# Kernel tuning notes

Measured on AMD Instinct MI355X. Metric: run time of the kernel, lower is better.

Reference implementation:

```python
import jax, jax.numpy as jnp
import numpy as np

HEAD = 16
EMB = 1024
D_K = EMB // HEAD


def setup_inputs() -> dict:
    key = jax.random.key(0)
    ks = jax.random.split(key, 11)
    B, S, E = 2, 2048, EMB
    scale = 1.0 / np.sqrt(E)
    inp = {
        "query": jax.random.normal(ks[0], (B, S, E), jnp.float32),
        "key": jax.random.normal(ks[1], (B, S, E), jnp.float32),
        "value": jax.random.normal(ks[2], (B, S, E), jnp.float32),
        "Wq": jax.random.normal(ks[3], (E, E), jnp.float32) * scale,
        "bq": jnp.zeros((E,), jnp.float32),
        "Wk": jax.random.normal(ks[4], (E, E), jnp.float32) * scale,
        "bk": jnp.zeros((E,), jnp.float32),
        "Wv": jax.random.normal(ks[5], (E, E), jnp.float32) * scale,
        "bv": jnp.zeros((E,), jnp.float32),
        "Wo": jax.random.normal(ks[6], (E, E), jnp.float32) * scale,
        "bo": jnp.zeros((E,), jnp.float32),
    }
    return inp


def reference(query, key, value, Wq, bq, Wk, bk, Wv, bv, Wo, bo):
    B, S, E = query.shape
    # 3 input projections, split into heads: [B, H, S, d_k]
    def proj(x, W, b):
        return (x @ W.T + b).reshape(B, S, HEAD, D_K).transpose(0, 2, 1, 3)

    q = proj(query, Wq, bq)
    k = proj(key, Wk, bk)
    v = proj(value, Wv, bv)

    # scaled dot-product attention (full matrix, as in original)
    scores = jnp.einsum("bhqd,bhkd->bhqk", q, k) / jnp.sqrt(jnp.float32(D_K))
    attn = jax.nn.softmax(scores, axis=-1)  # dropout in eval mode = identity
    x = jnp.einsum("bhqk,bhkd->bhqd", attn, v)

    # merge heads and output projection
    x = x.transpose(0, 2, 1, 3).reshape(B, S, E)
    return x @ Wo.T + bo
```

## Files before the change

kernel.cpp:

```cpp
#include <hip/hip_runtime.h>
#include <hip/hip_bf16.h>
#include <math.h>


constexpr int Sn = 2048;
constexpr int En = 1024;
constexpr int Hn = 16;
constexpr int Dk = 64;
constexpr int Kn = 1024;
constexpr size_t WSZ = 1048576;
constexpr size_t TSZ = 4194304;
constexpr int PST = 72;

#define QSCALE 0.18033688011112042f

typedef __bf16 bf16x8 __attribute__((ext_vector_type(8)));
typedef float  f32x4  __attribute__((ext_vector_type(4)));

union U16 { uint4 u; bf16x8 v; __hip_bfloat16 h[8]; };
union U8  { uint2 u; __hip_bfloat162 h2[2]; __hip_bfloat16 h[4]; };

__device__ inline U16 cvt8f(const float* __restrict__ p) {
    float4 a = *(const float4*)p;
    float4 b = *(const float4*)(p + 4);
    U16 r;
    r.h[0] = __float2bfloat16(a.x); r.h[1] = __float2bfloat16(a.y);
    r.h[2] = __float2bfloat16(a.z); r.h[3] = __float2bfloat16(a.w);
    r.h[4] = __float2bfloat16(b.x); r.h[5] = __float2bfloat16(b.y);
    r.h[6] = __float2bfloat16(b.z); r.h[7] = __float2bfloat16(b.w);
    return r;
}

__device__ inline void gload16(const __hip_bfloat16* g, __hip_bfloat16* l) {
    __builtin_amdgcn_global_load_lds(
        (const __attribute__((address_space(1))) void*)g,
        (__attribute__((address_space(3))) void*)l, 16, 0, 0);
}

template<int ROWS, int NW>
__device__ inline void stage_tile(const __hip_bfloat16* __restrict__ src, int ld,
                                  __hip_bfloat16* lds, int w, int lane) {
    int l8 = lane >> 3;
    int g = (lane & 7) ^ (l8 & 7);
    #pragma unroll
    for (int j = 0; j < ROWS / (8 * NW); ++j) {
        int c = j * NW + w;
        gload16(src + (size_t)(c * 8 + l8) * ld + g * 8, lds + c * 512);
    }
}

__global__ __launch_bounds__(256)
void cvt_w(const float* __restrict__ w0, const float* __restrict__ w1,
           const float* __restrict__ w2, const float* __restrict__ w3,
           __hip_bfloat16* __restrict__ dst)
{
    int y = blockIdx.y;
    const float* src = (y == 0) ? w0 : (y == 1) ? w1 : (y == 2) ? w2 : w3;
    size_t i = ((size_t)blockIdx.x * 256 + threadIdx.x) * 8;
    U16 r = cvt8f(src + i);
    *(uint4*)&dst[(size_t)y * WSZ + i] = r.u;
}

__global__ __launch_bounds__(256)
void cvt_x3(const float* __restrict__ q, const float* __restrict__ k,
            const float* __restrict__ v, __hip_bfloat16* __restrict__ dst)
{
    int z = blockIdx.y;
    const float* src = (z == 0) ? q : (z == 1) ? k : v;
    size_t i = ((size_t)blockIdx.x * 256 + threadIdx.x) * 8;
    U16 r = cvt8f(src + i);
    *(uint4*)&dst[(size_t)z * TSZ + i] = r.u;
}

template<int NT>
__device__ inline void gemm_core(const __hip_bfloat16* __restrict__ Ab,
                                 const __hip_bfloat16* __restrict__ Wb,
                                 __hip_bfloat16* As, __hip_bfloat16* Bs,
                                 f32x4 (&acc)[2][NT], int w, int lane)
{
    const int l15 = lane & 15, lg = lane >> 4, l7 = lane & 7;
    const int wm = (w & 1) * 32, wn = (w >> 1) * (NT * 16);
    const int coff0 = (lg ^ l7) * 8;
    const int coff1 = ((4 + lg) ^ l7) * 8;

    #pragma unroll
    for (int i = 0; i < 2; ++i)
        #pragma unroll
        for (int j = 0; j < NT; ++j) acc[i][j] = {0.f, 0.f, 0.f, 0.f};

    for (int k0 = 0; k0 < Kn; k0 += 64) {
        stage_tile<64, 4>(Ab + k0, Kn, As, w, lane);
        stage_tile<NT * 32, 4>(Wb + k0, Kn, Bs, w, lane);
        __syncthreads();

        U16 af[2][2], bf[NT][2];
        #pragma unroll
        for (int mt = 0; mt < 2; ++mt) {
            int r = (wm + mt * 16 + l15) * 64;
            af[mt][0].u = *(const uint4*)&As[r + coff0];
            af[mt][1].u = *(const uint4*)&As[r + coff1];
        }
        #pragma unroll
        for (int nt = 0; nt < NT; ++nt) {
            int r = (wn + nt * 16 + l15) * 64;
            bf[nt][0].u = *(const uint4*)&Bs[r + coff0];
            bf[nt][1].u = *(const uint4*)&Bs[r + coff1];
        }
        #pragma unroll
        for (int mt = 0; mt < 2; ++mt)
            #pragma unroll
            for (int nt = 0; nt < NT; ++nt) {
                acc[mt][nt] = __builtin_amdgcn_mfma_f32_16x16x32_bf16(af[mt][0].v, bf[nt][0].v, acc[mt][nt], 0, 0, 0);
                acc[mt][nt] = __builtin_amdgcn_mfma_f32_16x16x32_bf16(af[mt][1].v, bf[nt][1].v, acc[mt][nt], 0, 0, 0);
            }
        __syncthreads();
    }
}

__global__ __launch_bounds__(256)
void gemm_qkv(const __hip_bfloat16* __restrict__ X, const __hip_bfloat16* __restrict__ Wall,
              const float* __restrict__ bq, const float* __restrict__ bk,
              const float* __restrict__ bv, __hip_bfloat16* __restrict__ outbase)
{
    __shared__ __align__(16) __hip_bfloat16 As[64 * 64];
    __shared__ __align__(16) __hip_bfloat16 Bs[128 * 64];

    const int tid = threadIdx.x, w = tid >> 6, lane = tid & 63;
    const int z = blockIdx.z;
    const int blockM = blockIdx.x * 64, blockN = blockIdx.y * 128;

    f32x4 acc[2][4];
    gemm_core<4>(X + (size_t)z * TSZ + (size_t)blockM * Kn,
                 Wall + (size_t)z * WSZ + (size_t)blockN * Kn,
                 As, Bs, acc, w, lane);

    const float scale = (z == 0) ? QSCALE : 1.0f;
    const float* bias = (z == 0) ? bq : (z == 1) ? bk : bv;
    __hip_bfloat16* out = outbase + (size_t)z * TSZ;

    const int l15 = lane & 15, lg = lane >> 4;
    const int wm = (w & 1) * 32, wn = (w >> 1) * 64;

    #pragma unroll
    for (int nt = 0; nt < 4; ++nt) {
        int n = blockN + wn + nt * 16 + l15;
        float bvn = bias[n] * scale;
        int h_ = n >> 6, d_ = n & 63;
        #pragma unroll
        for (int mt = 0; mt < 2; ++mt) {
            int m0 = blockM + wm + mt * 16 + lg * 4;
            int b_ = m0 >> 11, s_ = m0 & (Sn - 1);
            if (z < 2) {
                #pragma unroll
                for (int i = 0; i < 4; ++i)
                    out[(((size_t)b_ * Hn + h_) * Sn + s_ + i) * Dk + d_] =
                        __float2bfloat16(fmaf(acc[mt][nt][i], scale, bvn));
            } else {
                U8 pk;
                #pragma unroll
                for (int i = 0; i < 4; ++i)
                    pk.h[i] = __float2bfloat16(fmaf(acc[mt][nt][i], scale, bvn));
                *(uint2*)&out[(((size_t)b_ * Hn + h_) * Dk + d_) * Sn + s_] = pk.u;
            }
        }
    }
}

__global__ __launch_bounds__(256)
void gemm_out(const __hip_bfloat16* __restrict__ A, const __hip_bfloat16* __restrict__ W,
              const float* __restrict__ bias, float* __restrict__ out)
{
    __shared__ __align__(16) __hip_bfloat16 As[64 * 64];
    __shared__ __align__(16) __hip_bfloat16 Bs[64 * 64];

    const int tid = threadIdx.x, w = tid >> 6, lane = tid & 63;
    const int blockM = blockIdx.x * 64, blockN = blockIdx.y * 64;

    f32x4 acc[2][2];
    gemm_core<2>(A + (size_t)blockM * Kn, W + (size_t)blockN * Kn,
                 As, Bs, acc, w, lane);

    const int l15 = lane & 15, lg = lane >> 4;
    const int wm = (w & 1) * 32, wn = (w >> 1) * 32;

    #pragma unroll
    for (int nt = 0; nt < 2; ++nt) {
        int n = blockN + wn + nt * 16 + l15;
        float bvn = bias[n];
        #pragma unroll
        for (int mt = 0; mt < 2; ++mt) {
            int m0 = blockM + wm + mt * 16 + lg * 4;
            #pragma unroll
            for (int i = 0; i < 4; ++i)
                out[(size_t)(m0 + i) * Kn + n] = acc[mt][nt][i] + bvn;
        }
    }
}

__global__ __launch_bounds__(256)
void attn(const __hip_bfloat16* __restrict__ Q, const __hip_bfloat16* __restrict__ K,
          const __hip_bfloat16* __restrict__ Vt, __hip_bfloat16* __restrict__ X)
{
    __shared__ __align__(16) __hip_bfloat16 Ks[2][64 * 64];
    __shared__ __align__(16) __hip_bfloat16 Vts[2][64 * 64];
    __shared__ __align__(16) __hip_bfloat16 Ps[128 * PST];

    const int bh = blockIdx.y, q0 = blockIdx.x * 128;
    const int tid = threadIdx.x, w = tid >> 6, lane = tid & 63;
    const int l15 = lane & 15, lg = lane >> 4, l7 = lane & 7;
    const int coff0 = (lg ^ l7) * 8;
    const int coff1 = ((4 + lg) ^ l7) * 8;

    const __hip_bfloat16* Qb = Q  + (size_t)bh * Sn * Dk;
    const __hip_bfloat16* Kb = K  + (size_t)bh * Sn * Dk;
    const __hip_bfloat16* Vb = Vt + (size_t)bh * Dk * Sn;

    U16 aq[2][2];
    #pragma unroll
    for (int qt = 0; qt < 2; ++qt) {
        const __hip_bfloat16* qp = Qb + (size_t)(q0 + w * 32 + qt * 16 + l15) * Dk + lg * 8;
        aq[qt][0].u = *(const uint4*)qp;
        aq[qt][1].u = *(const uint4*)(qp + 32);
    }

    f32x4 o[2][4];
    float lpart[2];
    #pragma unroll
    for (int qt = 0; qt < 2; ++qt) {
        lpart[qt] = 0.f;
        #pragma unroll
        for (int dt = 0; dt < 4; ++dt) o[qt][dt] = {0.f, 0.f, 0.f, 0.f};
    }

    __hip_bfloat16* Pw = Ps + (w * 32) * PST;

    stage_tile<64, 4>(Kb, Dk, Ks[0], w, lane);
    stage_tile<64, 4>(Vb, Sn, Vts[0], w, lane);

    for (int t = 0; t < Sn / 64; ++t) {
        __syncthreads();
        const int cur = t & 1;
        if (t + 1 < Sn / 64) {
            stage_tile<64, 4>(Kb + (size_t)(t + 1) * 64 * Dk, Dk, Ks[cur ^ 1], w, lane);
            stage_tile<64, 4>(Vb + (t + 1) * 64, Sn, Vts[cur ^ 1], w, lane);
        }

        U16 kf[4][2];
        #pragma unroll
        for (int kt = 0; kt < 4; ++kt) {
            int r = (kt * 16 + l15) * 64;
            kf[kt][0].u = *(const uint4*)&Ks[cur][r + coff0];
            kf[kt][1].u = *(const uint4*)&Ks[cur][r + coff1];
        }
        #pragma unroll
        for (int kt = 0; kt < 4; ++kt)
            #pragma unroll
            for (int qt = 0; qt < 2; ++qt) {
                f32x4 s = {0.f, 0.f, 0.f, 0.f};
                s = __builtin_amdgcn_mfma_f32_16x16x32_bf16(kf[kt][0].v, aq[qt][0].v, s, 0, 0, 0);
                s = __builtin_amdgcn_mfma_f32_16x16x32_bf16(kf[kt][1].v, aq[qt][1].v, s, 0, 0, 0);
                float p0 = __builtin_amdgcn_exp2f(s[0]), p1 = __builtin_amdgcn_exp2f(s[1]);
                float p2 = __builtin_amdgcn_exp2f(s[2]), p3 = __builtin_amdgcn_exp2f(s[3]);
                lpart[qt] += (p0 + p1) + (p2 + p3);
                U8 pk;
                pk.h2[0] = __float22bfloat162_rn({p0, p1});
                pk.h2[1] = __float22bfloat162_rn({p2, p3});
                *(uint2*)&Pw[(qt * 16 + l15) * PST + kt * 16 + lg * 4] = pk.u;
            }

        U16 pf[2][2], vf[4][2];
        #pragma unroll
        for (int qt = 0; qt < 2; ++qt) {
            const __hip_bfloat16* pr = &Pw[(qt * 16 + l15) * PST + lg * 8];
            pf[qt][0].u = *(const uint4*)pr;
            pf[qt][1].u = *(const uint4*)(pr + 32);
        }
        #pragma unroll
        for (int dt = 0; dt < 4; ++dt) {
            int r = (dt * 16 + l15) * 64;
            vf[dt][0].u = *(const uint4*)&Vts[cur][r + coff0];
            vf[dt][1].u = *(const uint4*)&Vts[cur][r + coff1];
        }
        #pragma unroll
        for (int qt = 0; qt < 2; ++qt)
            #pragma unroll
            for (int dt = 0; dt < 4; ++dt) {
                o[qt][dt] = __builtin_amdgcn_mfma_f32_16x16x32_bf16(pf[qt][0].v, vf[dt][0].v, o[qt][dt], 0, 0, 0);
                o[qt][dt] = __builtin_amdgcn_mfma_f32_16x16x32_bf16(pf[qt][1].v, vf[dt][1].v, o[qt][dt], 0, 0, 0);
            }
    }

    float linv[2][4];
    #pragma unroll
    for (int qt = 0; qt < 2; ++qt) {
        float v = lpart[qt];
        v += __shfl_xor(v, 16, 64);
        v += __shfl_xor(v, 32, 64);
        #pragma unroll
        for (int i = 0; i < 4; ++i)
            linv[qt][i] = 1.f / __shfl(v, lg * 4 + i, 16);
    }

    int b_ = bh >> 4, h_ = bh & (Hn - 1);
    #pragma unroll
    for (int qt = 0; qt < 2; ++qt)
        #pragma unroll
        for (int i = 0; i < 4; ++i) {
            int sr = q0 + w * 32 + qt * 16 + lg * 4 + i;
            __hip_bfloat16* xp = X + ((size_t)(b_ * Sn + sr)) * En + h_ * Dk + l15;
            #pragma unroll
            for (int dt = 0; dt < 4; ++dt)
                xp[dt * 16] = __float2bfloat16(o[qt][dt][i] * linv[qt][i]);
        }
}

extern "C" void kernel_launch(void* const* d_in, const int* in_sizes, int n_in,
                              void* d_out, int out_size, void* d_ws, size_t ws_size,
                              hipStream_t stream)
{
    const float* query = (const float*)d_in[0];
    const float* key   = (const float*)d_in[1];
    const float* value = (const float*)d_in[2];
    const float* Wq = (const float*)d_in[3];
    const float* bq = (const float*)d_in[4];
    const float* Wk = (const float*)d_in[5];
    const float* bk = (const float*)d_in[6];
    const float* Wv = (const float*)d_in[7];
    const float* bv = (const float*)d_in[8];
    const float* Wo = (const float*)d_in[9];
    const float* bo = (const float*)d_in[10];
    float* out = (float*)d_out;

    __hip_bfloat16* xqkv = (__hip_bfloat16*)d_ws;
    __hip_bfloat16* Wbf  = xqkv + 3 * TSZ;
    __hip_bfloat16* QKVw = Wbf + 4 * WSZ;
    __hip_bfloat16* Xw   = xqkv;

    cvt_w<<<dim3(512, 4), 256, 0, stream>>>(Wq, Wk, Wv, Wo, Wbf);
    cvt_x3<<<dim3(2048, 3), 256, 0, stream>>>(query, key, value, xqkv);
    gemm_qkv<<<dim3(64, 8, 3), 256, 0, stream>>>(xqkv, Wbf, bq, bk, bv, QKVw);
    attn<<<dim3(Sn / 128, 32), 256, 0, stream>>>(QKVw, QKVw + TSZ, QKVw + 2 * TSZ, Xw);
    gemm_out<<<dim3(64, 16), 256, 0, stream>>>(Xw, Wbf + 3 * WSZ, bo, out);
}
```

Before: 222.8 us.

## Use 32x32 MFMA with register-resident P in attention; enlarge GEMM M tiles

```diff
diff --git a/kernel.cpp b/kernel.cpp
--- a/kernel.cpp
+++ b/kernel.cpp
@@ -10,15 +10,16 @@
 constexpr int Kn = 1024;
 constexpr size_t WSZ = 1048576;
 constexpr size_t TSZ = 4194304;
-constexpr int PST = 72;
 
 #define QSCALE 0.18033688011112042f
 
 typedef __bf16 bf16x8 __attribute__((ext_vector_type(8)));
 typedef float  f32x4  __attribute__((ext_vector_type(4)));
+typedef float  f32x16 __attribute__((ext_vector_type(16)));
 
 union U16 { uint4 u; bf16x8 v; __hip_bfloat16 h[8]; };
 union U8  { uint2 u; __hip_bfloat162 h2[2]; __hip_bfloat16 h[4]; };
+union U4  { unsigned u; __hip_bfloat162 h2; };
 
 __device__ inline U16 cvt8f(const float* __restrict__ p) {
     float4 a = *(const float4*)p;
@@ -72,30 +73,30 @@
     *(uint4*)&dst[(size_t)z * TSZ + i] = r.u;
 }
 
-template<int NT>
+template<int MT, int NT>
 __device__ inline void gemm_core(const __hip_bfloat16* __restrict__ Ab,
                                  const __hip_bfloat16* __restrict__ Wb,
                                  __hip_bfloat16* As, __hip_bfloat16* Bs,
-                                 f32x4 (&acc)[2][NT], int w, int lane)
+                                 f32x4 (&acc)[MT][NT], int w, int lane)
 {
     const int l15 = lane & 15, lg = lane >> 4, l7 = lane & 7;
-    const int wm = (w & 1) * 32, wn = (w >> 1) * (NT * 16);
+    const int wm = (w & 1) * (MT * 16), wn = (w >> 1) * (NT * 16);
     const int coff0 = (lg ^ l7) * 8;
     const int coff1 = ((4 + lg) ^ l7) * 8;
 
     #pragma unroll
-    for (int i = 0; i < 2; ++i)
+    for (int i = 0; i < MT; ++i)
         #pragma unroll
         for (int j = 0; j < NT; ++j) acc[i][j] = {0.f, 0.f, 0.f, 0.f};
 
     for (int k0 = 0; k0 < Kn; k0 += 64) {
-        stage_tile<64, 4>(Ab + k0, Kn, As, w, lane);
+        stage_tile<MT * 32, 4>(Ab + k0, Kn, As, w, lane);
         stage_tile<NT * 32, 4>(Wb + k0, Kn, Bs, w, lane);
         __syncthreads();
 
-        U16 af[2][2], bf[NT][2];
-        #pragma unroll
-        for (int mt = 0; mt < 2; ++mt) {
+        U16 af[MT][2], bf[NT][2];
+        #pragma unroll
+        for (int mt = 0; mt < MT; ++mt) {
             int r = (wm + mt * 16 + l15) * 64;
             af[mt][0].u = *(const uint4*)&As[r + coff0];
             af[mt][1].u = *(const uint4*)&As[r + coff1];
@@ -107,7 +108,7 @@
             bf[nt][1].u = *(const uint4*)&Bs[r + coff1];
         }
         #pragma unroll
-        for (int mt = 0; mt < 2; ++mt)
+        for (int mt = 0; mt < MT; ++mt)
             #pragma unroll
             for (int nt = 0; nt < NT; ++nt) {
                 acc[mt][nt] = __builtin_amdgcn_mfma_f32_16x16x32_bf16(af[mt][0].v, bf[nt][0].v, acc[mt][nt], 0, 0, 0);
@@ -122,24 +123,24 @@
               const float* __restrict__ bq, const float* __restrict__ bk,
               const float* __restrict__ bv, __hip_bfloat16* __restrict__ outbase)
 {
-    __shared__ __align__(16) __hip_bfloat16 As[64 * 64];
+    __shared__ __align__(16) __hip_bfloat16 As[128 * 64];
     __shared__ __align__(16) __hip_bfloat16 Bs[128 * 64];
 
     const int tid = threadIdx.x, w = tid >> 6, lane = tid & 63;
     const int z = blockIdx.z;
-    const int blockM = blockIdx.x * 64, blockN = blockIdx.y * 128;
-
-    f32x4 acc[2][4];
-    gemm_core<4>(X + (size_t)z * TSZ + (size_t)blockM * Kn,
-                 Wall + (size_t)z * WSZ + (size_t)blockN * Kn,
-                 As, Bs, acc, w, lane);
+    const int blockM = blockIdx.x * 128, blockN = blockIdx.y * 128;
+
+    f32x4 acc[4][4];
+    gemm_core<4, 4>(X + (size_t)z * TSZ + (size_t)blockM * Kn,
+                    Wall + (size_t)z * WSZ + (size_t)blockN * Kn,
+                    As, Bs, acc, w, lane);
 
     const float scale = (z == 0) ? QSCALE : 1.0f;
     const float* bias = (z == 0) ? bq : (z == 1) ? bk : bv;
     __hip_bfloat16* out = outbase + (size_t)z * TSZ;
 
     const int l15 = lane & 15, lg = lane >> 4;
-    const int wm = (w & 1) * 32, wn = (w >> 1) * 64;
+    const int wm = (w & 1) * 64, wn = (w >> 1) * 64;
 
     #pragma unroll
     for (int nt = 0; nt < 4; ++nt) {
@@ -147,7 +148,7 @@
         float bvn = bias[n] * scale;
         int h_ = n >> 6, d_ = n & 63;
         #pragma unroll
-        for (int mt = 0; mt < 2; ++mt) {
+        for (int mt = 0; mt < 4; ++mt) {
             int m0 = blockM + wm + mt * 16 + lg * 4;
             int b_ = m0 >> 11, s_ = m0 & (Sn - 1);
             if (z < 2) {
@@ -170,25 +171,25 @@
 void gemm_out(const __hip_bfloat16* __restrict__ A, const __hip_bfloat16* __restrict__ W,
               const float* __restrict__ bias, float* __restrict__ out)
 {
-    __shared__ __align__(16) __hip_bfloat16 As[64 * 64];
+    __shared__ __align__(16) __hip_bfloat16 As[128 * 64];
     __shared__ __align__(16) __hip_bfloat16 Bs[64 * 64];
 
     const int tid = threadIdx.x, w = tid >> 6, lane = tid & 63;
-    const int blockM = blockIdx.x * 64, blockN = blockIdx.y * 64;
-
-    f32x4 acc[2][2];
-    gemm_core<2>(A + (size_t)blockM * Kn, W + (size_t)blockN * Kn,
-                 As, Bs, acc, w, lane);
+    const int blockM = blockIdx.x * 128, blockN = blockIdx.y * 64;
+
+    f32x4 acc[4][2];
+    gemm_core<4, 2>(A + (size_t)blockM * Kn, W + (size_t)blockN * Kn,
+                    As, Bs, acc, w, lane);
 
     const int l15 = lane & 15, lg = lane >> 4;
-    const int wm = (w & 1) * 32, wn = (w >> 1) * 32;
+    const int wm = (w & 1) * 64, wn = (w >> 1) * 32;
 
     #pragma unroll
     for (int nt = 0; nt < 2; ++nt) {
         int n = blockN + wn + nt * 16 + l15;
         float bvn = bias[n];
         #pragma unroll
-        for (int mt = 0; mt < 2; ++mt) {
+        for (int mt = 0; mt < 4; ++mt) {
             int m0 = blockM + wm + mt * 16 + lg * 4;
             #pragma unroll
             for (int i = 0; i < 4; ++i)
@@ -203,36 +204,29 @@
 {
     __shared__ __align__(16) __hip_bfloat16 Ks[2][64 * 64];
     __shared__ __align__(16) __hip_bfloat16 Vts[2][64 * 64];
-    __shared__ __align__(16) __hip_bfloat16 Ps[128 * PST];
 
     const int bh = blockIdx.y, q0 = blockIdx.x * 128;
     const int tid = threadIdx.x, w = tid >> 6, lane = tid & 63;
-    const int l15 = lane & 15, lg = lane >> 4, l7 = lane & 7;
-    const int coff0 = (lg ^ l7) * 8;
-    const int coff1 = ((4 + lg) ^ l7) * 8;
+    const int l31 = lane & 31, hi = lane >> 5;
 
     const __hip_bfloat16* Qb = Q  + (size_t)bh * Sn * Dk;
     const __hip_bfloat16* Kb = K  + (size_t)bh * Sn * Dk;
     const __hip_bfloat16* Vb = Vt + (size_t)bh * Dk * Sn;
 
-    U16 aq[2][2];
-    #pragma unroll
-    for (int qt = 0; qt < 2; ++qt) {
-        const __hip_bfloat16* qp = Qb + (size_t)(q0 + w * 32 + qt * 16 + l15) * Dk + lg * 8;
-        aq[qt][0].u = *(const uint4*)qp;
-        aq[qt][1].u = *(const uint4*)(qp + 32);
-    }
-
-    f32x4 o[2][4];
-    float lpart[2];
-    #pragma unroll
-    for (int qt = 0; qt < 2; ++qt) {
-        lpart[qt] = 0.f;
-        #pragma unroll
-        for (int dt = 0; dt < 4; ++dt) o[qt][dt] = {0.f, 0.f, 0.f, 0.f};
-    }
-
-    __hip_bfloat16* Pw = Ps + (w * 32) * PST;
+    U16 qf[4];
+    {
+        const __hip_bfloat16* qp = Qb + (size_t)(q0 + w * 32 + l31) * Dk + hi * 8;
+        #pragma unroll
+        for (int d0t = 0; d0t < 4; ++d0t)
+            qf[d0t].u = *(const uint4*)(qp + d0t * 16);
+    }
+
+    f32x16 o[2];
+    #pragma unroll
+    for (int dt = 0; dt < 2; ++dt)
+        #pragma unroll
+        for (int r = 0; r < 16; ++r) o[dt][r] = 0.f;
+    float lpart = 0.f;
 
     stage_tile<64, 4>(Kb, Dk, Ks[0], w, lane);
     stage_tile<64, 4>(Vb, Sn, Vts[0], w, lane);
@@ -245,73 +239,81 @@
             stage_tile<64, 4>(Vb + (t + 1) * 64, Sn, Vts[cur ^ 1], w, lane);
         }
 
-        U16 kf[4][2];
-        #pragma unroll
-        for (int kt = 0; kt < 4; ++kt) {
-            int r = (kt * 16 + l15) * 64;
-            kf[kt][0].u = *(const uint4*)&Ks[cur][r + coff0];
-            kf[kt][1].u = *(const uint4*)&Ks[cur][r + coff1];
-        }
-        #pragma unroll
-        for (int kt = 0; kt < 4; ++kt)
-            #pragma unroll
-            for (int qt = 0; qt < 2; ++qt) {
-                f32x4 s = {0.f, 0.f, 0.f, 0.f};
-                s = __builtin_amdgcn_mfma_f32_16x16x32_bf16(kf[kt][0].v, aq[qt][0].v, s, 0, 0, 0);
-                s = __builtin_amdgcn_mfma_f32_16x16x32_bf16(kf[kt][1].v, aq[qt][1].v, s, 0, 0, 0);
-                float p0 = __builtin_amdgcn_exp2f(s[0]), p1 = __builtin_amdgcn_exp2f(s[1]);
-                float p2 = __builtin_amdgcn_exp2f(s[2]), p3 = __builtin_amdgcn_exp2f(s[3]);
-                lpart[qt] += (p0 + p1) + (p2 + p3);
-                U8 pk;
-                pk.h2[0] = __float22bfloat162_rn({p0, p1});
-                pk.h2[1] = __float22bfloat162_rn({p2, p3});
-                *(uint2*)&Pw[(qt * 16 + l15) * PST + kt * 16 + lg * 4] = pk.u;
-            }
-
-        U16 pf[2][2], vf[4][2];
-        #pragma unroll
-        for (int qt = 0; qt < 2; ++qt) {
-            const __hip_bfloat16* pr = &Pw[(qt * 16 + l15) * PST + lg * 8];
-            pf[qt][0].u = *(const uint4*)pr;
-            pf[qt][1].u = *(const uint4*)(pr + 32);
-        }
-        #pragma unroll
-        for (int dt = 0; dt < 4; ++dt) {
-            int r = (dt * 16 + l15) * 64;
-            vf[dt][0].u = *(const uint4*)&Vts[cur][r + coff0];
-            vf[dt][1].u = *(const uint4*)&Vts[cur][r + coff1];
-        }
-        #pragma unroll
-        for (int qt = 0; qt < 2; ++qt)
-            #pragma unroll
-            for (int dt = 0; dt < 4; ++dt) {
-                o[qt][dt] = __builtin_amdgcn_mfma_f32_16x16x32_bf16(pf[qt][0].v, vf[dt][0].v, o[qt][dt], 0, 0, 0);
-                o[qt][dt] = __builtin_amdgcn_mfma_f32_16x16x32_bf16(pf[qt][1].v, vf[dt][1].v, o[qt][dt], 0, 0, 0);
-            }
-    }
-
-    float linv[2][4];
-    #pragma unroll
-    for (int qt = 0; qt < 2; ++qt) {
-        float v = lpart[qt];
-        v += __shfl_xor(v, 16, 64);
-        v += __shfl_xor(v, 32, 64);
-        #pragma unroll
-        for (int i = 0; i < 4; ++i)
-            linv[qt][i] = 1.f / __shfl(v, lg * 4 + i, 16);
+        f32x16 st[2];
+        #pragma unroll
+        for (int kt = 0; kt < 2; ++kt)
+            #pragma unroll
+            for (int r = 0; r < 16; ++r) st[kt][r] = 0.f;
+
+        #pragma unroll
+        for (int d0t = 0; d0t < 4; ++d0t) {
+            #pragma unroll
+            for (int kt = 0; kt < 2; ++kt) {
+                int r = kt * 32 + l31;
+                int col = (((d0t * 2 + hi)) ^ (r & 7)) * 8;
+                U16 kf; kf.u = *(const uint4*)&Ks[cur][r * 64 + col];
+                st[kt] = __builtin_amdgcn_mfma_f32_32x32x16_bf16(kf.v, qf[d0t].v, st[kt], 0, 0, 0);
+            }
+        }
+
+        uint4 pa[4];
+        #pragma unroll
+        for (int kt = 0; kt < 2; ++kt) {
+            float pv[16];
+            #pragma unroll
+            for (int r = 0; r < 16; ++r) pv[r] = __builtin_amdgcn_exp2f(st[kt][r]);
+            float s01 = (pv[0] + pv[1]) + (pv[2] + pv[3]);
+            float s23 = (pv[4] + pv[5]) + (pv[6] + pv[7]);
+            float s45 = (pv[8] + pv[9]) + (pv[10] + pv[11]);
+            float s67 = (pv[12] + pv[13]) + (pv[14] + pv[15]);
+            lpart += (s01 + s23) + (s45 + s67);
+
+            uint wv[8];
+            #pragma unroll
+            for (int m2 = 0; m2 < 8; ++m2) {
+                U4 pk; pk.h2 = __float22bfloat162_rn({pv[2 * m2], pv[2 * m2 + 1]});
+                wv[m2] = pk.u;
+            }
+            asm volatile("v_permlane32_swap_b32 %0, %1" : "+v"(wv[0]), "+v"(wv[2]));
+            asm volatile("v_permlane32_swap_b32 %0, %1" : "+v"(wv[1]), "+v"(wv[3]));
+            asm volatile("v_permlane32_swap_b32 %0, %1" : "+v"(wv[4]), "+v"(wv[6]));
+            asm volatile("v_permlane32_swap_b32 %0, %1" : "+v"(wv[5]), "+v"(wv[7]));
+            pa[kt * 2 + 0] = make_uint4(wv[0], wv[1], wv[2], wv[3]);
+            pa[kt * 2 + 1] = make_uint4(wv[4], wv[5], wv[6], wv[7]);
+        }
+
+        #pragma unroll
+        for (int k0t = 0; k0t < 4; ++k0t) {
+            U16 pau; pau.u = pa[k0t];
+            #pragma unroll
+            for (int dt = 0; dt < 2; ++dt) {
+                int r = dt * 32 + l31;
+                int col = (((k0t * 2 + hi)) ^ (r & 7)) * 8;
+                U16 vf; vf.u = *(const uint4*)&Vts[cur][r * 64 + col];
+                o[dt] = __builtin_amdgcn_mfma_f32_32x32x16_bf16(pau.v, vf.v, o[dt], 0, 0, 0);
+            }
+        }
+    }
+
+    lpart += __shfl_xor(lpart, 32, 64);
+    float linv = 1.f / lpart;
+
+    float li[16];
+    #pragma unroll
+    for (int r = 0; r < 16; ++r) {
+        int qr = (r & 3) + 8 * (r >> 2) + 4 * hi;
+        li[r] = __shfl(linv, qr, 64);
     }
 
     int b_ = bh >> 4, h_ = bh & (Hn - 1);
     #pragma unroll
-    for (int qt = 0; qt < 2; ++qt)
-        #pragma unroll
-        for (int i = 0; i < 4; ++i) {
-            int sr = q0 + w * 32 + qt * 16 + lg * 4 + i;
-            __hip_bfloat16* xp = X + ((size_t)(b_ * Sn + sr)) * En + h_ * Dk + l15;
-            #pragma unroll
-            for (int dt = 0; dt < 4; ++dt)
-                xp[dt * 16] = __float2bfloat16(o[qt][dt][i] * linv[qt][i]);
-        }
+    for (int r = 0; r < 16; ++r) {
+        int qr = (r & 3) + 8 * (r >> 2) + 4 * hi;
+        int sr = q0 + w * 32 + qr;
+        __hip_bfloat16* xp = X + ((size_t)(b_ * Sn + sr)) * En + h_ * Dk + l31;
+        xp[0]  = __float2bfloat16(o[0][r] * li[r]);
+        xp[32] = __float2bfloat16(o[1][r] * li[r]);
+    }
 }
 
 extern "C" void kernel_launch(void* const* d_in, const int* in_sizes, int n_in,
@@ -338,7 +340,7 @@
 
     cvt_w<<<dim3(512, 4), 256, 0, stream>>>(Wq, Wk, Wv, Wo, Wbf);
     cvt_x3<<<dim3(2048, 3), 256, 0, stream>>>(query, key, value, xqkv);
-    gemm_qkv<<<dim3(64, 8, 3), 256, 0, stream>>>(xqkv, Wbf, bq, bk, bv, QKVw);
+    gemm_qkv<<<dim3(32, 8, 3), 256, 0, stream>>>(xqkv, Wbf, bq, bk, bv, QKVw);
     attn<<<dim3(Sn / 128, 32), 256, 0, stream>>>(QKVw, QKVw + TSZ, QKVw + 2 * TSZ, Xw);
-    gemm_out<<<dim3(64, 16), 256, 0, stream>>>(Xw, Wbf + 3 * WSZ, bo, out);
-}
+    gemm_out<<<dim3(32, 16), 256, 0, stream>>>(Xw, Wbf + 3 * WSZ, bo, out);
+}
```

Measured after the change: 231.1 us. 3.7% more time.
